# Kernel optimization log

Hardware: AMD Instinct MI355X
Metric: run time of the kernel (lower is better)

Reference implementation:

```python
import jax, jax.numpy as jnp
import numpy as np

N, IN_DIM, OUT_DIM, NUM_EXPERTS, TOP_K = 8192, 1024, 1024, 8, 2


def setup_inputs() -> dict:
    key = jax.random.key(0)
    ks = jax.random.split(key, 5)
    s_in = 1.0 / np.sqrt(IN_DIM)
    x = jax.random.normal(ks[0], (N, IN_DIM), dtype=jnp.float32)
    # per-expert Linear weights: [E, in, out] (torch Linear weight is [out,in]; we store transposed)
    W = jax.random.uniform(ks[1], (NUM_EXPERTS, IN_DIM, OUT_DIM), jnp.float32, -s_in, s_in)
    b = jax.random.uniform(ks[2], (NUM_EXPERTS, OUT_DIM), jnp.float32, -s_in, s_in)
    Wg = jax.random.uniform(ks[3], (IN_DIM, NUM_EXPERTS), jnp.float32, -s_in, s_in)
    bg = jax.random.uniform(ks[4], (NUM_EXPERTS,), jnp.float32, -s_in, s_in)
    return {"x": x, "W": W, "b": b, "Wg": Wg, "bg": bg}


def reference(x, W, b, Wg, bg):
    # gating scores [N, E]
    scores = x @ Wg + bg
    # top-k mask
    _, top_idx = jax.lax.top_k(scores, TOP_K)  # [N, k]
    mask = jnp.zeros_like(scores).at[jnp.arange(x.shape[0])[:, None], top_idx].set(1.0)
    masked = jnp.where(mask == 0, -jnp.inf, scores)
    gating_weights = jax.nn.softmax(masked, axis=-1)  # [N, E]
    # all-expert linear: [N, E, out]
    expert_outputs = jnp.einsum('ni,eio->neo', x, W) + b
    # weighted combine over experts
    return jnp.einsum('ne,neo->no', gating_weights, expert_outputs)
```

## Files before the change

kernel.cpp:

```cpp
#include <hip/hip_runtime.h>

#define N_TOK 8192
#define IN_DIM 1024
#define OUT_DIM 1024
#define NE 8
#define TILE_SH 12288

typedef short short8 __attribute__((ext_vector_type(8)));
typedef float f32x4 __attribute__((ext_vector_type(4)));
typedef ushort ushort4v __attribute__((ext_vector_type(4)));

__device__ __forceinline__ ushort f2bf(float f) {
    union { float f; unsigned u; } v; v.f = f;
    unsigned u = v.u;
    unsigned r = (u + 0x7fffu + ((u >> 16) & 1u)) >> 16;
    return (ushort)r;
}

__device__ __forceinline__ float bf2f(short s) {
    union { unsigned u; float f; } v;
    v.u = ((unsigned)(unsigned short)s) << 16;
    return v.f;
}

__device__ __forceinline__ void gl_lds16(const short* g, short* l) {
    __builtin_amdgcn_global_load_lds(
        (const __attribute__((address_space(1))) unsigned int*)g,
        (__attribute__((address_space(3))) unsigned int*)l, 16, 0, 0);
}

__global__ __launch_bounds__(256) void prep(const float* __restrict__ x,
                                            const float* __restrict__ Wg,
                                            const float* __restrict__ bg,
                                            const float* __restrict__ W,
                                            short* __restrict__ xb,
                                            short* __restrict__ wt,
                                            unsigned* __restrict__ choice,
                                            float2* __restrict__ wts) {
    __shared__ ushort tile[32][33];
    int bid = blockIdx.x;
    if (bid < 2048) {
        int wid = threadIdx.x >> 6, lane = threadIdx.x & 63;
        int tok = bid * 4 + wid;
        const float* xr = x + (size_t)tok * IN_DIM;
        short* xbr = xb + (size_t)tok * IN_DIM;
        float acc[8];
        #pragma unroll
        for (int e = 0; e < 8; ++e) acc[e] = 0.f;
        #pragma unroll
        for (int it = 0; it < 4; ++it) {
            int j = it * 256 + lane * 4;
            float4 v = *(const float4*)(xr + j);
            ushort4v o;
            o[0] = f2bf(v.x); o[1] = f2bf(v.y); o[2] = f2bf(v.z); o[3] = f2bf(v.w);
            *(ushort4v*)(xbr + j) = o;
            #pragma unroll
            for (int r = 0; r < 4; ++r) {
                float xv = (r == 0) ? v.x : (r == 1) ? v.y : (r == 2) ? v.z : v.w;
                float4 wa = *(const float4*)(Wg + (size_t)(j + r) * 8);
                float4 wb = *(const float4*)(Wg + (size_t)(j + r) * 8 + 4);
                acc[0] += xv * wa.x; acc[1] += xv * wa.y;
                acc[2] += xv * wa.z; acc[3] += xv * wa.w;
                acc[4] += xv * wb.x; acc[5] += xv * wb.y;
                acc[6] += xv * wb.z; acc[7] += xv * wb.w;
            }
        }
        #pragma unroll
        for (int e = 0; e < 8; ++e)
            #pragma unroll
            for (int off = 32; off; off >>= 1)
                acc[e] += __shfl_xor(acc[e], off, 64);
        if (lane == 0) {
            float s[8];
            #pragma unroll
            for (int e = 0; e < 8; ++e) s[e] = acc[e] + bg[e];
            int i0 = 0;
            #pragma unroll
            for (int e = 1; e < 8; ++e) if (s[e] > s[i0]) i0 = e;
            int i1 = (i0 == 0) ? 1 : 0;
            #pragma unroll
            for (int e = 0; e < 8; ++e) if (e != i0 && s[e] > s[i1]) i1 = e;
            float e0 = 1.f, e1 = __expf(s[i1] - s[i0]);
            float inv = 1.f / (e0 + e1);
            choice[tok] = (unsigned)i0 | ((unsigned)i1 << 8);
            wts[tok] = make_float2(e0 * inv, e1 * inv);
        }
    } else {
        int id = bid - 2048;
        int nt = id & 31, kt = (id >> 5) & 31, e = id >> 10;
        int t = threadIdx.x;
        int r = t >> 3;
        int c4 = (t & 7) * 4;
        const float4 v = *(const float4*)(W + (((size_t)e * 1024 + kt * 32 + r) * 1024) + nt * 32 + c4);
        tile[c4 + 0][r] = f2bf(v.x);
        tile[c4 + 1][r] = f2bf(v.y);
        tile[c4 + 2][r] = f2bf(v.z);
        tile[c4 + 3][r] = f2bf(v.w);
        __syncthreads();
        int n = t >> 3, kq = (t & 7) * 4;
        ushort4v o;
        o[0] = tile[n][kq + 0]; o[1] = tile[n][kq + 1];
        o[2] = tile[n][kq + 2]; o[3] = tile[n][kq + 3];
        *(ushort4v*)(wt + (((size_t)e * 1024 + nt * 32 + n) * 1024) + kt * 32 + kq) = o;
    }
}

__global__ __launch_bounds__(1024) void bucket(const unsigned* __restrict__ choice,
                                               int* __restrict__ counts,
                                               int* __restrict__ entries,
                                               int* __restrict__ inv0,
                                               int* __restrict__ inv1) {
    int e = blockIdx.x;
    int t = threadIdx.x;
    int wid = t >> 6, lane = t & 63;
    __shared__ int wsum[16];
    unsigned c[8];
    #pragma unroll
    for (int chunk = 0; chunk < 8; ++chunk) c[chunk] = choice[chunk * 1024 + t];
    int base = 0;
    #pragma unroll
    for (int chunk = 0; chunk < 8; ++chunk) {
        int tok = chunk * 1024 + t;
        int which = ((int)(c[chunk] & 255u) == e) ? 0
                  : (((int)((c[chunk] >> 8) & 255u) == e) ? 1 : -1);
        unsigned long long m = __ballot(which >= 0);
        if (lane == 0) wsum[wid] = __popcll(m);
        __syncthreads();
        int woff = base;
        #pragma unroll
        for (int i = 0; i < 16; ++i) if (i < wid) woff += wsum[i];
        int tot = 0;
        #pragma unroll
        for (int i = 0; i < 16; ++i) tot += wsum[i];
        if (which >= 0) {
            int rank = __popcll(m & ((1ull << lane) - 1ull));
            int idx = woff + rank;
            entries[e * N_TOK + idx] = tok;
            if (which == 0) inv0[tok] = idx; else inv1[tok] = idx;
        }
        base += tot;
        __syncthreads();
    }
    if (t == 0) counts[e] = base;
}

__global__ __launch_bounds__(256, 2) void moe_gemm(const short* __restrict__ xb,
                                                   const short* __restrict__ wt,
                                                   const float* __restrict__ bias,
                                                   const int* __restrict__ counts,
                                                   const int* __restrict__ entries,
                                                   short* __restrict__ ys) {
    int lin = blockIdx.x;
    int e = lin & 7;
    int inner = lin >> 3;
    int ct = inner & 3, rt = inner >> 2;
    int cnt = counts[e];
    if (rt * 128 >= cnt) return;
    int rows = min(128, cnt - rt * 128);
    int base_e = 0;
    #pragma unroll
    for (int i = 0; i < NE; ++i) base_e += (i < e) ? counts[i] : 0;

    __shared__ __align__(16) short lds[3 * TILE_SH];
    __shared__ int tok_sh[128];

    int t = threadIdx.x, wid = t >> 6, lane = t & 63;
    int ebase = e * N_TOK + rt * 128;
    if (t < 128) tok_sh[t] = (t < rows) ? entries[ebase + t] : entries[ebase];
    __syncthreads();

    int chunkoff = (((t & 3) ^ ((t >> 2) & 3)) * 8);
    const short* asrc0 = xb + (size_t)tok_sh[t >> 2] * IN_DIM + chunkoff;
    const short* asrc1 = xb + (size_t)tok_sh[64 + (t >> 2)] * IN_DIM + chunkoff;
    const short* bsrc0 = wt + ((size_t)e * OUT_DIM + ct * 256 + (t >> 2)) * IN_DIM + chunkoff;
    const short* bsrc1 = bsrc0 + (size_t)64 * IN_DIM;
    const short* bsrc2 = bsrc0 + (size_t)128 * IN_DIM;
    const short* bsrc3 = bsrc0 + (size_t)192 * IN_DIM;
    int dst8 = t * 8;

    int wr = wid >> 1, wc = wid & 1;
    int frow = lane & 15, fslot = lane >> 4;
    int rslot = (fslot ^ (frow & 3)) * 8;
    int aoff[4], boff[8];
    #pragma unroll
    for (int mi = 0; mi < 4; ++mi) aoff[mi] = (wr * 64 + mi * 16 + frow) * 32 + rslot;
    #pragma unroll
    for (int ni = 0; ni < 8; ++ni) boff[ni] = (wc * 128 + ni * 16 + frow) * 32 + rslot;

    f32x4 acc[4][8];
    #pragma unroll
    for (int mi = 0; mi < 4; ++mi)
        #pragma unroll
        for (int ni = 0; ni < 8; ++ni) acc[mi][ni] = (f32x4)(0.0f);

    short8 caf[4], cbf[8];

#define STAGE(BUF, KT)                                                        \
    {                                                                         \
        short* nb = lds + (BUF) * TILE_SH;                                    \
        int nk = (KT) * 32;                                                   \
        gl_lds16(asrc0 + nk, nb + dst8);                                      \
        gl_lds16(asrc1 + nk, nb + 2048 + dst8);                               \
        gl_lds16(bsrc0 + nk, nb + 4096 + dst8);                               \
        gl_lds16(bsrc1 + nk, nb + 6144 + dst8);                               \
        gl_lds16(bsrc2 + nk, nb + 8192 + dst8);                               \
        gl_lds16(bsrc3 + nk, nb + 10240 + dst8);                              \
    }

#define LOADFRAGS(BUF)                                                        \
    {                                                                         \
        const short* Ab = lds + (BUF) * TILE_SH;                              \
        const short* Bb = Ab + 4096;                                          \
        _Pragma("unroll")                                                     \
        for (int mi = 0; mi < 4; ++mi) caf[mi] = *(const short8*)(Ab + aoff[mi]); \
        _Pragma("unroll")                                                     \
        for (int ni = 0; ni < 8; ++ni) cbf[ni] = *(const short8*)(Bb + boff[ni]); \
        __builtin_amdgcn_sched_barrier(0);                                    \
    }

#define GITER(NXTBUF, STGBUF, KTN, VN, DO_STAGE, DO_TAIL)                     \
    {                                                                         \
        if (DO_STAGE) STAGE(STGBUF, KTN);                                     \
        __builtin_amdgcn_s_barrier();                                         \
        __builtin_amdgcn_s_setprio(1);                                        \
        _Pragma("unroll")                                                     \
        for (int mi = 0; mi < 4; ++mi)                                        \
            _Pragma("unroll")                                                 \
            for (int ni = 0; ni < 8; ++ni)                                    \
                acc[mi][ni] = __builtin_amdgcn_mfma_f32_16x16x32_bf16(        \
                    caf[mi], cbf[ni], acc[mi][ni], 0, 0, 0);                  \
        __builtin_amdgcn_s_setprio(0);                                        \
        asm volatile("s_waitcnt vmcnt(" VN ")" ::: "memory");                 \
        __builtin_amdgcn_s_barrier();                                         \
        if (DO_TAIL) LOADFRAGS(NXTBUF);                                       \
    }

    STAGE(0, 0);
    STAGE(1, 1);
    asm volatile("s_waitcnt vmcnt(6)" ::: "memory");
    __builtin_amdgcn_s_barrier();
    LOADFRAGS(0);

    for (int kt = 0; kt < 30; kt += 3) {
        GITER(1, 2, kt + 2, "6", 1, 1);
        GITER(2, 0, kt + 3, "6", 1, 1);
        GITER(0, 1, kt + 4, "6", 1, 1);
    }
    GITER(1, 0, 0, "0", 0, 1);
    GITER(0, 0, 0, "0", 0, 0);

#undef GITER
#undef LOADFRAGS
#undef STAGE

    __syncthreads();
    short* ep = lds;
    const float* be = bias + (size_t)e * OUT_DIM;
    #pragma unroll
    for (int ni = 0; ni < 8; ++ni) {
        int col = wc * 128 + ni * 16 + frow;
        float bv = be[ct * 256 + col];
        #pragma unroll
        for (int mi = 0; mi < 4; ++mi) {
            int rb_ = wr * 64 + mi * 16 + fslot * 4;
            #pragma unroll
            for (int r = 0; r < 4; ++r)
                ep[(rb_ + r) * 268 + col] = (short)f2bf(acc[mi][ni][r] + bv);
        }
    }
    __syncthreads();
    #pragma unroll
    for (int k = 0; k < 16; ++k) {
        int f = t + k * 256;
        int row = f >> 5, cw = f & 31;
        if (row < rows) {
            short8 v = *(const short8*)(ep + row * 268 + cw * 8);
            *(short8*)(ys + ((size_t)(base_e + rt * 128 + row)) * OUT_DIM
                       + ct * 256 + cw * 8) = v;
        }
    }
}

__global__ __launch_bounds__(256) void combine(const short* __restrict__ ys,
                                               const unsigned* __restrict__ choice,
                                               const float2* __restrict__ wts,
                                               const int* __restrict__ inv0,
                                               const int* __restrict__ inv1,
                                               const int* __restrict__ counts,
                                               float* __restrict__ out) {
    __shared__ int bases[8];
    if (threadIdx.x < 8) {
        int s = 0;
        #pragma unroll
        for (int i = 0; i < 8; ++i) s += (i < (int)threadIdx.x) ? counts[i] : 0;
        bases[threadIdx.x] = s;
    }
    __syncthreads();
    int tok = blockIdx.x * 2 + (threadIdx.x >> 7);
    int c8 = (threadIdx.x & 127) * 8;
    unsigned ch = choice[tok];
    float2 w = wts[tok];
    int p0 = bases[ch & 255u] + inv0[tok];
    int p1 = bases[(ch >> 8) & 255u] + inv1[tok];
    short8 a = *(const short8*)(ys + (size_t)p0 * OUT_DIM + c8);
    short8 b = *(const short8*)(ys + (size_t)p1 * OUT_DIM + c8);
    float* op = out + (size_t)tok * OUT_DIM + c8;
    float4 o0, o1;
    o0.x = w.x * bf2f(a[0]) + w.y * bf2f(b[0]);
    o0.y = w.x * bf2f(a[1]) + w.y * bf2f(b[1]);
    o0.z = w.x * bf2f(a[2]) + w.y * bf2f(b[2]);
    o0.w = w.x * bf2f(a[3]) + w.y * bf2f(b[3]);
    o1.x = w.x * bf2f(a[4]) + w.y * bf2f(b[4]);
    o1.y = w.x * bf2f(a[5]) + w.y * bf2f(b[5]);
    o1.z = w.x * bf2f(a[6]) + w.y * bf2f(b[6]);
    o1.w = w.x * bf2f(a[7]) + w.y * bf2f(b[7]);
    *(float4*)op = o0;
    *(float4*)(op + 4) = o1;
}

extern "C" void kernel_launch(void* const* d_in, const int* in_sizes, int n_in,
                              void* d_out, int out_size, void* d_ws, size_t ws_size,
                              hipStream_t stream) {
    const float* x  = (const float*)d_in[0];
    const float* W  = (const float*)d_in[1];
    const float* b  = (const float*)d_in[2];
    const float* Wg = (const float*)d_in[3];
    const float* bg = (const float*)d_in[4];
    float* out = (float*)d_out;

    char* ws = (char*)d_ws;
    short* xb        = (short*)(ws);
    short* wt        = (short*)(ws + 16777216);
    unsigned* choice = (unsigned*)(ws + 33554432);
    float2* wts      = (float2*)(ws + 33587200);
    int* inv0        = (int*)(ws + 33652736);
    int* inv1        = (int*)(ws + 33685504);
    int* entries     = (int*)(ws + 33718272);
    int* counts      = (int*)(ws + 34242560);
    short* ys        = (short*)(ws + 34242624);

    prep<<<10240, 256, 0, stream>>>(x, Wg, bg, W, xb, wt, choice, wts);
    bucket<<<8, 1024, 0, stream>>>(choice, counts, entries, inv0, inv1);
    moe_gemm<<<2048, 256, 0, stream>>>(xb, wt, b, counts, entries, ys);
    combine<<<4096, 256, 0, stream>>>(ys, choice, wts, inv0, inv1, counts, out);
}
```

Measured before the change: 113.2 us.

## Shrink GEMM tile to 128x128 with double buffering and higher occupancy

Result: no change. 114.0 us (+0.7%).

```diff
diff --git a/kernel.cpp b/kernel.cpp
--- a/kernel.cpp
+++ b/kernel.cpp
@@ -4,7 +4,7 @@
 #define IN_DIM 1024
 #define OUT_DIM 1024
 #define NE 8
-#define TILE_SH 12288
+#define BUFSH 8192
 
 typedef short short8 __attribute__((ext_vector_type(8)));
 typedef float f32x4 __attribute__((ext_vector_type(4)));
@@ -144,7 +144,7 @@
     if (t == 0) counts[e] = base;
 }
 
-__global__ __launch_bounds__(256, 2) void moe_gemm(const short* __restrict__ xb,
+__global__ __launch_bounds__(256, 4) void moe_gemm(const short* __restrict__ xb,
                                                    const short* __restrict__ wt,
                                                    const float* __restrict__ bias,
                                                    const int* __restrict__ counts,
@@ -153,7 +153,7 @@
     int lin = blockIdx.x;
     int e = lin & 7;
     int inner = lin >> 3;
-    int ct = inner & 3, rt = inner >> 2;
+    int ct = inner & 7, rt = inner >> 3;
     int cnt = counts[e];
     if (rt * 128 >= cnt) return;
     int rows = min(128, cnt - rt * 128);
@@ -161,7 +161,7 @@
     #pragma unroll
     for (int i = 0; i < NE; ++i) base_e += (i < e) ? counts[i] : 0;
 
-    __shared__ __align__(16) short lds[3 * TILE_SH];
+    __shared__ __align__(16) short lds[16896];
     __shared__ int tok_sh[128];
 
     int t = threadIdx.x, wid = t >> 6, lane = t & 63;
@@ -169,85 +169,78 @@
     if (t < 128) tok_sh[t] = (t < rows) ? entries[ebase + t] : entries[ebase];
     __syncthreads();
 
-    int chunkoff = (((t & 3) ^ ((t >> 2) & 3)) * 8);
-    const short* asrc0 = xb + (size_t)tok_sh[t >> 2] * IN_DIM + chunkoff;
-    const short* asrc1 = xb + (size_t)tok_sh[64 + (t >> 2)] * IN_DIM + chunkoff;
-    const short* bsrc0 = wt + ((size_t)e * OUT_DIM + ct * 256 + (t >> 2)) * IN_DIM + chunkoff;
+    int r0 = t >> 2;
+    int chunkoff = (((t & 3) ^ (r0 & 3)) * 8);
+    const short* asrc0 = xb + (size_t)tok_sh[r0] * IN_DIM + chunkoff;
+    const short* asrc1 = xb + (size_t)tok_sh[64 + r0] * IN_DIM + chunkoff;
+    const short* bsrc0 = wt + ((size_t)e * OUT_DIM + ct * 128 + r0) * IN_DIM + chunkoff;
     const short* bsrc1 = bsrc0 + (size_t)64 * IN_DIM;
-    const short* bsrc2 = bsrc0 + (size_t)128 * IN_DIM;
-    const short* bsrc3 = bsrc0 + (size_t)192 * IN_DIM;
     int dst8 = t * 8;
 
     int wr = wid >> 1, wc = wid & 1;
     int frow = lane & 15, fslot = lane >> 4;
-    int rslot = (fslot ^ (frow & 3)) * 8;
-    int aoff[4], boff[8];
+    int rslot = ((fslot ^ (frow & 3)) * 8);
+    int aoff[4], boff[4];
     #pragma unroll
     for (int mi = 0; mi < 4; ++mi) aoff[mi] = (wr * 64 + mi * 16 + frow) * 32 + rslot;
     #pragma unroll
-    for (int ni = 0; ni < 8; ++ni) boff[ni] = (wc * 128 + ni * 16 + frow) * 32 + rslot;
-
-    f32x4 acc[4][8];
+    for (int ni = 0; ni < 4; ++ni) boff[ni] = 4096 + (wc * 64 + ni * 16 + frow) * 32 + rslot;
+
+    f32x4 acc[4][4];
     #pragma unroll
     for (int mi = 0; mi < 4; ++mi)
         #pragma unroll
-        for (int ni = 0; ni < 8; ++ni) acc[mi][ni] = (f32x4)(0.0f);
-
-    short8 caf[4], cbf[8];
+        for (int ni = 0; ni < 4; ++ni) acc[mi][ni] = (f32x4)(0.0f);
+
+    short8 caf[4], cbf[4];
 
 #define STAGE(BUF, KT)                                                        \
     {                                                                         \
-        short* nb = lds + (BUF) * TILE_SH;                                    \
+        short* nb = lds + (BUF) * BUFSH;                                      \
         int nk = (KT) * 32;                                                   \
         gl_lds16(asrc0 + nk, nb + dst8);                                      \
         gl_lds16(asrc1 + nk, nb + 2048 + dst8);                               \
         gl_lds16(bsrc0 + nk, nb + 4096 + dst8);                               \
         gl_lds16(bsrc1 + nk, nb + 6144 + dst8);                               \
-        gl_lds16(bsrc2 + nk, nb + 8192 + dst8);                               \
-        gl_lds16(bsrc3 + nk, nb + 10240 + dst8);                              \
     }
 
 #define LOADFRAGS(BUF)                                                        \
     {                                                                         \
-        const short* Ab = lds + (BUF) * TILE_SH;                              \
-        const short* Bb = Ab + 4096;                                          \
+        const short* Ab = lds + (BUF) * BUFSH;                                \
         _Pragma("unroll")                                                     \
         for (int mi = 0; mi < 4; ++mi) caf[mi] = *(const short8*)(Ab + aoff[mi]); \
         _Pragma("unroll")                                                     \
-        for (int ni = 0; ni < 8; ++ni) cbf[ni] = *(const short8*)(Bb + boff[ni]); \
+        for (int ni = 0; ni < 4; ++ni) cbf[ni] = *(const short8*)(Ab + boff[ni]); \
         __builtin_amdgcn_sched_barrier(0);                                    \
     }
 
-#define GITER(NXTBUF, STGBUF, KTN, VN, DO_STAGE, DO_TAIL)                     \
+#define GITER(CUR, KTN, DO_STAGE, DO_TAIL)                                    \
     {                                                                         \
-        if (DO_STAGE) STAGE(STGBUF, KTN);                                     \
-        __builtin_amdgcn_s_barrier();                                         \
+        if (DO_STAGE) STAGE((CUR) ^ 1, KTN);                                  \
         __builtin_amdgcn_s_setprio(1);                                        \
         _Pragma("unroll")                                                     \
         for (int mi = 0; mi < 4; ++mi)                                        \
             _Pragma("unroll")                                                 \
-            for (int ni = 0; ni < 8; ++ni)                                    \
+            for (int ni = 0; ni < 4; ++ni)                                    \
                 acc[mi][ni] = __builtin_amdgcn_mfma_f32_16x16x32_bf16(        \
                     caf[mi], cbf[ni], acc[mi][ni], 0, 0, 0);                  \
         __builtin_amdgcn_s_setprio(0);                                        \
-        asm volatile("s_waitcnt vmcnt(" VN ")" ::: "memory");                 \
+        asm volatile("s_waitcnt vmcnt(0)" ::: "memory");                      \
         __builtin_amdgcn_s_barrier();                                         \
-        if (DO_TAIL) LOADFRAGS(NXTBUF);                                       \
+        if (DO_TAIL) LOADFRAGS((CUR) ^ 1);                                    \
     }
 
     STAGE(0, 0);
-    STAGE(1, 1);
-    asm volatile("s_waitcnt vmcnt(6)" ::: "memory");
+    asm volatile("s_waitcnt vmcnt(0)" ::: "memory");
     __builtin_amdgcn_s_barrier();
     LOADFRAGS(0);
 
-    for (int kt = 0; kt < 30; kt += 3) {
-        GITER(1, 2, kt + 2, "6", 1, 1);
-        GITER(2, 0, kt + 3, "6", 1, 1);
-        GITER(0, 1, kt + 4, "6", 1, 1);
-    }
-    GITER(1, 0, 0, "0", 0, 1);
-    GITER(0, 0, 0, "0", 0, 0);
+    for (int kt2 = 0; kt2 < 15; ++kt2) {
+        GITER(0, 2 * kt2 + 1, 1, 1);
+        GITER(1, 2 * kt2 + 2, 1, 1);
+    }
+    GITER(0, 31, 1, 1);
+    GITER(1, 0, 0, 0);
 
 #undef GITER
 #undef LOADFRAGS
@@ -257,26 +250,26 @@
     short* ep = lds;
     const float* be = bias + (size_t)e * OUT_DIM;
     #pragma unroll
-    for (int ni = 0; ni < 8; ++ni) {
-        int col = wc * 128 + ni * 16 + frow;
-        float bv = be[ct * 256 + col];
+    for (int ni = 0; ni < 4; ++ni) {
+        int col = wc * 64 + ni * 16 + frow;
+        float bv = be[ct * 128 + col];
         #pragma unroll
         for (int mi = 0; mi < 4; ++mi) {
             int rb_ = wr * 64 + mi * 16 + fslot * 4;
             #pragma unroll
             for (int r = 0; r < 4; ++r)
-                ep[(rb_ + r) * 268 + col] = (short)f2bf(acc[mi][ni][r] + bv);
+                ep[(rb_ + r) * 132 + col] = (short)f2bf(acc[mi][ni][r] + bv);
         }
     }
     __syncthreads();
     #pragma unroll
-    for (int k = 0; k < 16; ++k) {
+    for (int k = 0; k < 8; ++k) {
         int f = t + k * 256;
-        int row = f >> 5, cw = f & 31;
+        int row = f >> 4, cw = f & 15;
         if (row < rows) {
-            short8 v = *(const short8*)(ep + row * 268 + cw * 8);
+            short8 v = *(const short8*)(ep + row * 132 + cw * 8);
             *(short8*)(ys + ((size_t)(base_e + rt * 128 + row)) * OUT_DIM
-                       + ct * 256 + cw * 8) = v;
+                       + ct * 128 + cw * 8) = v;
         }
     }
 }
@@ -341,6 +334,6 @@
 
     prep<<<10240, 256, 0, stream>>>(x, Wg, bg, W, xb, wt, choice, wts);
     bucket<<<8, 1024, 0, stream>>>(choice, counts, entries, inv0, inv1);
-    moe_gemm<<<2048, 256, 0, stream>>>(xb, wt, b, counts, entries, ys);
+    moe_gemm<<<4096, 256, 0, stream>>>(xb, wt, b, counts, entries, ys);
     combine<<<4096, 256, 0, stream>>>(ys, choice, wts, inv0, inv1, counts, out);
 }
```

## Fuse expert combine into GEMM epilogue with per-token claim flags

Applied to the files above, without the earlier changes.

Measured after the change: 329.7 us. 2.91x slower.

```diff
diff --git a/kernel.cpp b/kernel.cpp
--- a/kernel.cpp
+++ b/kernel.cpp
@@ -15,12 +15,6 @@
     unsigned u = v.u;
     unsigned r = (u + 0x7fffu + ((u >> 16) & 1u)) >> 16;
     return (ushort)r;
-}
-
-__device__ __forceinline__ float bf2f(short s) {
-    union { unsigned u; float f; } v;
-    v.u = ((unsigned)(unsigned short)s) << 16;
-    return v.f;
 }
 
 __device__ __forceinline__ void gl_lds16(const short* g, short* l) {
@@ -106,10 +100,10 @@
 }
 
 __global__ __launch_bounds__(1024) void bucket(const unsigned* __restrict__ choice,
+                                               const float2* __restrict__ wts,
                                                int* __restrict__ counts,
                                                int* __restrict__ entries,
-                                               int* __restrict__ inv0,
-                                               int* __restrict__ inv1) {
+                                               float* __restrict__ entw) {
     int e = blockIdx.x;
     int t = threadIdx.x;
     int wid = t >> 6, lane = t & 63;
@@ -136,7 +130,8 @@
             int rank = __popcll(m & ((1ull << lane) - 1ull));
             int idx = woff + rank;
             entries[e * N_TOK + idx] = tok;
-            if (which == 0) inv0[tok] = idx; else inv1[tok] = idx;
+            float2 w = wts[tok];
+            entw[e * N_TOK + idx] = (which == 0) ? w.x : w.y;
         }
         base += tot;
         __syncthreads();
@@ -149,7 +144,9 @@
                                                    const float* __restrict__ bias,
                                                    const int* __restrict__ counts,
                                                    const int* __restrict__ entries,
-                                                   short* __restrict__ ys) {
+                                                   const float* __restrict__ entw,
+                                                   int* __restrict__ flags,
+                                                   float* __restrict__ out) {
     int lin = blockIdx.x;
     int e = lin & 7;
     int inner = lin >> 3;
@@ -157,16 +154,18 @@
     int cnt = counts[e];
     if (rt * 128 >= cnt) return;
     int rows = min(128, cnt - rt * 128);
-    int base_e = 0;
-    #pragma unroll
-    for (int i = 0; i < NE; ++i) base_e += (i < e) ? counts[i] : 0;
 
     __shared__ __align__(16) short lds[3 * TILE_SH];
     __shared__ int tok_sh[128];
+    __shared__ float w_sh[128];
+    __shared__ int cl_sh[128];
 
     int t = threadIdx.x, wid = t >> 6, lane = t & 63;
     int ebase = e * N_TOK + rt * 128;
-    if (t < 128) tok_sh[t] = (t < rows) ? entries[ebase + t] : entries[ebase];
+    if (t < 128) {
+        tok_sh[t] = (t < rows) ? entries[ebase + t] : entries[ebase];
+        w_sh[t] = (t < rows) ? entw[ebase + t] : 0.f;
+    }
     __syncthreads();
 
     int chunkoff = (((t & 3) ^ ((t >> 2) & 3)) * 8);
@@ -253,69 +252,52 @@
 #undef LOADFRAGS
 #undef STAGE
 
+    if (t < 128) cl_sh[t] = (t < rows) ? (atomicCAS(&flags[tok_sh[t] * 4 + ct], 0, 1) == 0) : 0;
     __syncthreads();
-    short* ep = lds;
-    const float* be = bias + (size_t)e * OUT_DIM;
+
+    const float* be = bias + (size_t)e * OUT_DIM + ct * 256;
     #pragma unroll
     for (int ni = 0; ni < 8; ++ni) {
         int col = wc * 128 + ni * 16 + frow;
-        float bv = be[ct * 256 + col];
+        float bv = be[col];
         #pragma unroll
         for (int mi = 0; mi < 4; ++mi) {
             int rb_ = wr * 64 + mi * 16 + fslot * 4;
             #pragma unroll
-            for (int r = 0; r < 4; ++r)
-                ep[(rb_ + r) * 268 + col] = (short)f2bf(acc[mi][ni][r] + bv);
+            for (int r = 0; r < 4; ++r) {
+                int rl = rb_ + r;
+                if (rl < rows && cl_sh[rl])
+                    out[(size_t)tok_sh[rl] * OUT_DIM + ct * 256 + col] =
+                        w_sh[rl] * (acc[mi][ni][r] + bv);
+            }
         }
     }
     __syncthreads();
-    #pragma unroll
-    for (int k = 0; k < 16; ++k) {
-        int f = t + k * 256;
-        int row = f >> 5, cw = f & 31;
-        if (row < rows) {
-            short8 v = *(const short8*)(ep + row * 268 + cw * 8);
-            *(short8*)(ys + ((size_t)(base_e + rt * 128 + row)) * OUT_DIM
-                       + ct * 256 + cw * 8) = v;
-        }
-    }
-}
-
-__global__ __launch_bounds__(256) void combine(const short* __restrict__ ys,
-                                               const unsigned* __restrict__ choice,
-                                               const float2* __restrict__ wts,
-                                               const int* __restrict__ inv0,
-                                               const int* __restrict__ inv1,
-                                               const int* __restrict__ counts,
-                                               float* __restrict__ out) {
-    __shared__ int bases[8];
-    if (threadIdx.x < 8) {
-        int s = 0;
-        #pragma unroll
-        for (int i = 0; i < 8; ++i) s += (i < (int)threadIdx.x) ? counts[i] : 0;
-        bases[threadIdx.x] = s;
-    }
+    __threadfence();
+    if (t < 128 && t < rows && cl_sh[t]) atomicExch(&flags[tok_sh[t] * 4 + ct], 2);
+    if (t < 128 && t < rows && !cl_sh[t]) {
+        while (atomicAdd(&flags[tok_sh[t] * 4 + ct], 0) != 2)
+            __builtin_amdgcn_s_sleep(1);
+    }
+    __threadfence();
     __syncthreads();
-    int tok = blockIdx.x * 2 + (threadIdx.x >> 7);
-    int c8 = (threadIdx.x & 127) * 8;
-    unsigned ch = choice[tok];
-    float2 w = wts[tok];
-    int p0 = bases[ch & 255u] + inv0[tok];
-    int p1 = bases[(ch >> 8) & 255u] + inv1[tok];
-    short8 a = *(const short8*)(ys + (size_t)p0 * OUT_DIM + c8);
-    short8 b = *(const short8*)(ys + (size_t)p1 * OUT_DIM + c8);
-    float* op = out + (size_t)tok * OUT_DIM + c8;
-    float4 o0, o1;
-    o0.x = w.x * bf2f(a[0]) + w.y * bf2f(b[0]);
-    o0.y = w.x * bf2f(a[1]) + w.y * bf2f(b[1]);
-    o0.z = w.x * bf2f(a[2]) + w.y * bf2f(b[2]);
-    o0.w = w.x * bf2f(a[3]) + w.y * bf2f(b[3]);
-    o1.x = w.x * bf2f(a[4]) + w.y * bf2f(b[4]);
-    o1.y = w.x * bf2f(a[5]) + w.y * bf2f(b[5]);
-    o1.z = w.x * bf2f(a[6]) + w.y * bf2f(b[6]);
-    o1.w = w.x * bf2f(a[7]) + w.y * bf2f(b[7]);
-    *(float4*)op = o0;
-    *(float4*)(op + 4) = o1;
+    #pragma unroll
+    for (int ni = 0; ni < 8; ++ni) {
+        int col = wc * 128 + ni * 16 + frow;
+        float bv = be[col];
+        #pragma unroll
+        for (int mi = 0; mi < 4; ++mi) {
+            int rb_ = wr * 64 + mi * 16 + fslot * 4;
+            #pragma unroll
+            for (int r = 0; r < 4; ++r) {
+                int rl = rb_ + r;
+                if (rl < rows && !cl_sh[rl]) {
+                    float* p = out + (size_t)tok_sh[rl] * OUT_DIM + ct * 256 + col;
+                    *p += w_sh[rl] * (acc[mi][ni][r] + bv);
+                }
+            }
+        }
+    }
 }
 
 extern "C" void kernel_launch(void* const* d_in, const int* in_sizes, int n_in,
@@ -333,14 +315,14 @@
     short* wt        = (short*)(ws + 16777216);
     unsigned* choice = (unsigned*)(ws + 33554432);
     float2* wts      = (float2*)(ws + 33587200);
-    int* inv0        = (int*)(ws + 33652736);
-    int* inv1        = (int*)(ws + 33685504);
     int* entries     = (int*)(ws + 33718272);
+    float* entw      = (float*)(ws + 33980416);
     int* counts      = (int*)(ws + 34242560);
-    short* ys        = (short*)(ws + 34242624);
+    int* flags       = (int*)(ws + 34242624);
+
+    hipMemsetAsync(flags, 0, (size_t)N_TOK * 4 * sizeof(int), stream);
 
     prep<<<10240, 256, 0, stream>>>(x, Wg, bg, W, xb, wt, choice, wts);
-    bucket<<<8, 1024, 0, stream>>>(choice, counts, entries, inv0, inv1);
-    moe_gemm<<<2048, 256, 0, stream>>>(xb, wt, b, counts, entries, ys);
-    combine<<<4096, 256, 0, stream>>>(ys, choice, wts, inv0, inv1, counts, out);
-}
+    bucket<<<8, 1024, 0, stream>>>(choice, wts, counts, entries, entw);
+    moe_gemm<<<2048, 256, 0, stream>>>(xb, wt, b, counts, entries, entw, flags, out);
+}
```
